# Kernel optimization log

Measured on AMD Instinct MI355X. Metric: run time of the kernel, lower is better.

The kernel has to match this reference:

```python
import jax, jax.numpy as jnp
import numpy as np

N_NODES = 50000
N_EDGES = 800000
D_IN = 64
D_OUT = 64
D_U = 64


def setup_inputs() -> dict:
    key = jax.random.key(0)
    ks = jax.random.split(key, 6)
    x = jax.random.normal(ks[0], (N_NODES, D_IN), dtype=jnp.float32)
    edge_index = jax.random.randint(ks[1], (2, N_EDGES), 0, N_NODES, dtype=jnp.int64)
    edge_weight = jax.random.uniform(ks[2], (N_EDGES,), dtype=jnp.float32)
    u = jax.random.normal(ks[3], (N_NODES, D_U), dtype=jnp.float32)
    # xavier-uniform-like init for W and A
    limW = float(np.sqrt(6.0 / (D_IN + D_OUT)))
    W = jax.random.uniform(ks[4], (D_IN, D_OUT), minval=-limW, maxval=limW, dtype=jnp.float32)
    limA = float(np.sqrt(6.0 / (D_U + D_OUT)))
    A = jax.random.uniform(ks[5], (D_U, D_OUT), minval=-limA, maxval=limA, dtype=jnp.float32)
    bias = jnp.zeros((D_OUT,), dtype=jnp.float32)
    return {"x": x, "edge_index": edge_index, "edge_weight": edge_weight,
            "u": u, "W": W, "A": A, "bias": bias}


def reference(x, edge_index, edge_weight, u, W, A, bias):
    # Non-negative weights via softplus (input-convex constraint)
    W_nn = jax.nn.softplus(W)                      # [D_in, D_out]
    # Transform all nodes once, then gather per edge (equivalent to x[src] @ W per edge)
    h = x @ W_nn                                   # [N, D_out]
    src, dst = edge_index[0], edge_index[1]
    msgs = h[src] * edge_weight[:, None]           # [E, D_out]
    out = jax.ops.segment_sum(msgs, dst, num_segments=x.shape[0])  # [N, D_out]
    out = out + u @ jax.nn.softplus(A) + bias
    return jax.nn.relu(out)
```

## Files before the change

### kernel.cpp

```cpp
#include <hip/hip_runtime.h>

#define NN 50000
#define NE 800000
#define DD 64
#define CAP 64
#define XPAD 68

__global__ void k_softplus(const float* __restrict__ W, const float* __restrict__ A,
                           float* __restrict__ Wnn, float* __restrict__ Ann) {
    int i = blockIdx.x * blockDim.x + threadIdx.x;
    if (i < DD * DD) {
        float w = W[i];
        Wnn[i] = fmaxf(w, 0.f) + log1pf(expf(-fabsf(w)));
        float a = A[i];
        Ann[i] = fmaxf(a, 0.f) + log1pf(expf(-fabsf(a)));
    }
}

__global__ __launch_bounds__(256, 4) void k_transform(
    const float* __restrict__ x, const float* __restrict__ u,
    const float* __restrict__ Wnn, const float* __restrict__ Ann,
    const float* __restrict__ bias,
    float* __restrict__ h, float* __restrict__ base) {
    __shared__ float sW[DD * DD];
    __shared__ float sx[64 * XPAD];

    const int tid = threadIdx.x;
    const int tr = tid >> 4;
    const int tc = tid & 15;
    const int r0 = blockIdx.x * 64;
    const int phase = blockIdx.y;
    const float* __restrict__ in = phase ? u : x;
    const float* __restrict__ wm = phase ? Ann : Wnn;
    float* __restrict__ op = phase ? base : h;
    const int nrow = min(64, NN - r0);

    {
        const float4* w4 = (const float4*)wm;
        float4* sw4 = (float4*)sW;
        #pragma unroll
        for (int i = tid; i < DD * DD / 4; i += 256) sw4[i] = w4[i];
    }
    {
        const float4* x4 = (const float4*)(in + (size_t)r0 * DD);
        const int n4 = nrow * (DD / 4);
        #pragma unroll
        for (int i = tid; i < 64 * (DD / 4); i += 256) {
            float4 v = (i < n4) ? x4[i] : make_float4(0.f, 0.f, 0.f, 0.f);
            *(float4*)&sx[(i >> 4) * XPAD + (i & 15) * 4] = v;
        }
    }
    __syncthreads();

    float4 bv = make_float4(0.f, 0.f, 0.f, 0.f);
    if (phase) bv = *(const float4*)&bias[tc * 4];
    float4 acc[4] = {bv, bv, bv, bv};

    #pragma unroll 4
    for (int k4 = 0; k4 < DD / 4; ++k4) {
        float4 w0 = *(const float4*)&sW[(k4 * 4 + 0) * DD + tc * 4];
        float4 w1 = *(const float4*)&sW[(k4 * 4 + 1) * DD + tc * 4];
        float4 w2 = *(const float4*)&sW[(k4 * 4 + 2) * DD + tc * 4];
        float4 w3 = *(const float4*)&sW[(k4 * 4 + 3) * DD + tc * 4];
        #pragma unroll
        for (int i = 0; i < 4; ++i) {
            float4 xv = *(const float4*)&sx[(tr * 4 + i) * XPAD + k4 * 4];
            acc[i].x += xv.x * w0.x + xv.y * w1.x + xv.z * w2.x + xv.w * w3.x;
            acc[i].y += xv.x * w0.y + xv.y * w1.y + xv.z * w2.y + xv.w * w3.y;
            acc[i].z += xv.x * w0.z + xv.y * w1.z + xv.z * w2.z + xv.w * w3.z;
            acc[i].w += xv.x * w0.w + xv.y * w1.w + xv.z * w2.w + xv.w * w3.w;
        }
    }
    #pragma unroll
    for (int i = 0; i < 4; ++i) {
        int r = r0 + tr * 4 + i;
        if (r < NN) *(float4*)&op[(size_t)r * DD + tc * 4] = acc[i];
    }
}

__global__ __launch_bounds__(256) void k_scatter(
    const int* __restrict__ ei, const float* __restrict__ ew,
    int* __restrict__ cursor, float2* __restrict__ slots) {
    int e = blockIdx.x * 256 + threadIdx.x;
    if (e >= NE) return;
    int s = ei[e];
    int d = ei[NE + e];
    float w = ew[e];
    int pos = atomicAdd(&cursor[d], 1);
    if (pos < CAP) {
        float2 v;
        v.x = __int_as_float(s);
        v.y = w;
        slots[(size_t)d * CAP + pos] = v;
    }
}

__global__ __launch_bounds__(256) void k_apply(
    const int* __restrict__ cursor, const float2* __restrict__ slots,
    const float* __restrict__ h, float* __restrict__ out) {
    int wid = (blockIdx.x * 256 + threadIdx.x) >> 6;
    int lane = threadIdx.x & 63;
    if (wid >= NN) return;
    int deg = min(cursor[wid], CAP);
    const float2* sl = slots + (size_t)wid * CAP;
    float acc = 0.f;
    int i = 0;
    for (; i + 4 <= deg; i += 4) {
        float4 p0 = *(const float4*)(sl + i);
        float4 p1 = *(const float4*)(sl + i + 2);
        int s0 = __float_as_int(p0.x), s1 = __float_as_int(p0.z);
        int s2 = __float_as_int(p1.x), s3 = __float_as_int(p1.z);
        float h0 = h[(size_t)s0 * DD + lane];
        float h1 = h[(size_t)s1 * DD + lane];
        float h2 = h[(size_t)s2 * DD + lane];
        float h3 = h[(size_t)s3 * DD + lane];
        acc += h0 * p0.y + h1 * p0.w + h2 * p1.y + h3 * p1.w;
    }
    for (; i < deg; ++i) {
        float2 v = sl[i];
        acc += h[(size_t)__float_as_int(v.x) * DD + lane] * v.y;
    }
    size_t o = (size_t)wid * DD + lane;
    out[o] = fmaxf(out[o] + acc, 0.f);
}

extern "C" void kernel_launch(void* const* d_in, const int* in_sizes, int n_in,
                              void* d_out, int out_size, void* d_ws, size_t ws_size,
                              hipStream_t stream) {
    const float* x    = (const float*)d_in[0];
    const int*   ei   = (const int*)d_in[1];
    const float* ew   = (const float*)d_in[2];
    const float* u    = (const float*)d_in[3];
    const float* W    = (const float*)d_in[4];
    const float* A    = (const float*)d_in[5];
    const float* bias = (const float*)d_in[6];
    float* out = (float*)d_out;
    float* ws  = (float*)d_ws;

    float* Wnn    = ws;
    float* Ann    = ws + 4096;
    float* h      = ws + 8192;
    int*   cursor = (int*)(ws + 8192 + NN * DD);
    float2* slots = (float2*)(ws + 8192 + NN * DD + NN);

    hipMemsetAsync(cursor, 0, NN * sizeof(int), stream);
    k_softplus<<<(DD * DD + 255) / 256, 256, 0, stream>>>(W, A, Wnn, Ann);
    dim3 tg((NN + 63) / 64, 2);
    k_transform<<<tg, 256, 0, stream>>>(x, u, Wnn, Ann, bias, h, out);
    k_scatter<<<(NE + 255) / 256, 256, 0, stream>>>(ei, ew, cursor, slots);
    k_apply<<<(NN * 64 + 255) / 256, 256, 0, stream>>>(cursor, slots, h, out);
}
```

Before: 186.7 us.

## Fuse softplus, node transform and edge scatter into one kernel launch

Merges the softplus, the dense transform and the edge bucketing scatter into a single kernel. The first blocks do the scatter and the remaining blocks do the transform, with softplus computed inline while the weights load into shared memory. This removes two launches and the intermediate Wnn/Ann buffers, and lets the atomic-heavy scatter overlap with the compute-bound transform. In exchange every transform block recomputes softplus over 4096 weights, scatter blocks carry the 33KB static shared-memory footprint, and the apply kernel gets a tighter launch bound.

New measurement: 203.2 us. +8.8%, slower.

```diff
diff --git a/kernel.cpp b/kernel.cpp
--- a/kernel.cpp
+++ b/kernel.cpp
@@ -5,41 +5,60 @@
 #define DD 64
 #define CAP 64
 #define XPAD 68
+#define NBT 782
+#define NBS 3125
 
-__global__ void k_softplus(const float* __restrict__ W, const float* __restrict__ A,
-                           float* __restrict__ Wnn, float* __restrict__ Ann) {
-    int i = blockIdx.x * blockDim.x + threadIdx.x;
-    if (i < DD * DD) {
-        float w = W[i];
-        Wnn[i] = fmaxf(w, 0.f) + log1pf(expf(-fabsf(w)));
-        float a = A[i];
-        Ann[i] = fmaxf(a, 0.f) + log1pf(expf(-fabsf(a)));
-    }
-}
-
-__global__ __launch_bounds__(256, 4) void k_transform(
+__global__ __launch_bounds__(256, 4) void k_fused(
     const float* __restrict__ x, const float* __restrict__ u,
-    const float* __restrict__ Wnn, const float* __restrict__ Ann,
+    const float* __restrict__ W, const float* __restrict__ A,
     const float* __restrict__ bias,
+    const int* __restrict__ ei, const float* __restrict__ ew,
+    int* __restrict__ cursor, float2* __restrict__ slots,
     float* __restrict__ h, float* __restrict__ base) {
     __shared__ float sW[DD * DD];
     __shared__ float sx[64 * XPAD];
 
     const int tid = threadIdx.x;
+    int b = blockIdx.x;
+
+    if (b < NBS) {
+        int e = b * 256 + tid;
+        if (e < NE) {
+            int s = ei[e];
+            int d = ei[NE + e];
+            float w = ew[e];
+            int pos = atomicAdd(&cursor[d], 1);
+            if (pos < CAP) {
+                float2 v;
+                v.x = __int_as_float(s);
+                v.y = w;
+                slots[(size_t)d * CAP + pos] = v;
+            }
+        }
+        return;
+    }
+    b -= NBS;
+    const int phase = (b >= NBT) ? 1 : 0;
+    const int bx = phase ? b - NBT : b;
+    const float* __restrict__ in = phase ? u : x;
+    const float* __restrict__ wm = phase ? A : W;
+    float* __restrict__ op = phase ? base : h;
+    const int r0 = bx * 64;
+    const int nrow = min(64, NN - r0);
     const int tr = tid >> 4;
     const int tc = tid & 15;
-    const int r0 = blockIdx.x * 64;
-    const int phase = blockIdx.y;
-    const float* __restrict__ in = phase ? u : x;
-    const float* __restrict__ wm = phase ? Ann : Wnn;
-    float* __restrict__ op = phase ? base : h;
-    const int nrow = min(64, NN - r0);
 
     {
         const float4* w4 = (const float4*)wm;
-        float4* sw4 = (float4*)sW;
         #pragma unroll
-        for (int i = tid; i < DD * DD / 4; i += 256) sw4[i] = w4[i];
+        for (int i = tid; i < DD * DD / 4; i += 256) {
+            float4 v = w4[i];
+            v.x = fmaxf(v.x, 0.f) + log1pf(expf(-fabsf(v.x)));
+            v.y = fmaxf(v.y, 0.f) + log1pf(expf(-fabsf(v.y)));
+            v.z = fmaxf(v.z, 0.f) + log1pf(expf(-fabsf(v.z)));
+            v.w = fmaxf(v.w, 0.f) + log1pf(expf(-fabsf(v.w)));
+            *(float4*)&sW[i * 4] = v;
+        }
     }
     {
         const float4* x4 = (const float4*)(in + (size_t)r0 * DD);
@@ -78,24 +97,7 @@
     }
 }
 
-__global__ __launch_bounds__(256) void k_scatter(
-    const int* __restrict__ ei, const float* __restrict__ ew,
-    int* __restrict__ cursor, float2* __restrict__ slots) {
-    int e = blockIdx.x * 256 + threadIdx.x;
-    if (e >= NE) return;
-    int s = ei[e];
-    int d = ei[NE + e];
-    float w = ew[e];
-    int pos = atomicAdd(&cursor[d], 1);
-    if (pos < CAP) {
-        float2 v;
-        v.x = __int_as_float(s);
-        v.y = w;
-        slots[(size_t)d * CAP + pos] = v;
-    }
-}
-
-__global__ __launch_bounds__(256) void k_apply(
+__global__ __launch_bounds__(256, 8) void k_apply(
     const int* __restrict__ cursor, const float2* __restrict__ slots,
     const float* __restrict__ h, float* __restrict__ out) {
     int wid = (blockIdx.x * 256 + threadIdx.x) >> 6;
@@ -137,16 +139,12 @@
     float* out = (float*)d_out;
     float* ws  = (float*)d_ws;
 
-    float* Wnn    = ws;
-    float* Ann    = ws + 4096;
-    float* h      = ws + 8192;
-    int*   cursor = (int*)(ws + 8192 + NN * DD);
-    float2* slots = (float2*)(ws + 8192 + NN * DD + NN);
+    float*  h      = ws;
+    int*    cursor = (int*)(ws + NN * DD);
+    float2* slots  = (float2*)(ws + NN * DD + NN);
 
     hipMemsetAsync(cursor, 0, NN * sizeof(int), stream);
-    k_softplus<<<(DD * DD + 255) / 256, 256, 0, stream>>>(W, A, Wnn, Ann);
-    dim3 tg((NN + 63) / 64, 2);
-    k_transform<<<tg, 256, 0, stream>>>(x, u, Wnn, Ann, bias, h, out);
-    k_scatter<<<(NE + 255) / 256, 256, 0, stream>>>(ei, ew, cursor, slots);
+    k_fused<<<NBS + 2 * NBT, 256, 0, stream>>>(x, u, W, A, bias, ei, ew,
+                                               cursor, slots, h, out);
     k_apply<<<(NN * 64 + 255) / 256, 256, 0, stream>>>(cursor, slots, h, out);
 }
```

## Store transformed node features in bf16 and widen gather unrolling in apply

Applied to the files above, without the earlier changes.

The intermediate h matrix is now written as bf16 instead of fp32, which halves the bytes moved by the random per-edge gathers in the apply kernel. The apply loop is unrolled to 8 edges per iteration with vector slot loads and a 2-edge tail, and it gets a higher occupancy hint. The scatter kernel is launched before the transform, and the bias add is moved after the matmul. The cost is reduced precision in h, which adds rounding error to the aggregated messages.

Measured after the change: 183.8 us. About the same (-1.6%).

```diff
diff --git a/kernel.cpp b/kernel.cpp
--- a/kernel.cpp
+++ b/kernel.cpp
@@ -5,6 +5,15 @@
 #define DD 64
 #define CAP 64
 #define XPAD 68
+
+__device__ __forceinline__ unsigned short f2bf(float f) {
+    unsigned int b = __float_as_uint(f);
+    b += 0x7FFFu + ((b >> 16) & 1u);
+    return (unsigned short)(b >> 16);
+}
+__device__ __forceinline__ float bf2f(unsigned short h) {
+    return __uint_as_float(((unsigned int)h) << 16);
+}
 
 __global__ void k_softplus(const float* __restrict__ W, const float* __restrict__ A,
                            float* __restrict__ Wnn, float* __restrict__ Ann) {
@@ -14,67 +23,6 @@
         Wnn[i] = fmaxf(w, 0.f) + log1pf(expf(-fabsf(w)));
         float a = A[i];
         Ann[i] = fmaxf(a, 0.f) + log1pf(expf(-fabsf(a)));
-    }
-}
-
-__global__ __launch_bounds__(256, 4) void k_transform(
-    const float* __restrict__ x, const float* __restrict__ u,
-    const float* __restrict__ Wnn, const float* __restrict__ Ann,
-    const float* __restrict__ bias,
-    float* __restrict__ h, float* __restrict__ base) {
-    __shared__ float sW[DD * DD];
-    __shared__ float sx[64 * XPAD];
-
-    const int tid = threadIdx.x;
-    const int tr = tid >> 4;
-    const int tc = tid & 15;
-    const int r0 = blockIdx.x * 64;
-    const int phase = blockIdx.y;
-    const float* __restrict__ in = phase ? u : x;
-    const float* __restrict__ wm = phase ? Ann : Wnn;
-    float* __restrict__ op = phase ? base : h;
-    const int nrow = min(64, NN - r0);
-
-    {
-        const float4* w4 = (const float4*)wm;
-        float4* sw4 = (float4*)sW;
-        #pragma unroll
-        for (int i = tid; i < DD * DD / 4; i += 256) sw4[i] = w4[i];
-    }
-    {
-        const float4* x4 = (const float4*)(in + (size_t)r0 * DD);
-        const int n4 = nrow * (DD / 4);
-        #pragma unroll
-        for (int i = tid; i < 64 * (DD / 4); i += 256) {
-            float4 v = (i < n4) ? x4[i] : make_float4(0.f, 0.f, 0.f, 0.f);
-            *(float4*)&sx[(i >> 4) * XPAD + (i & 15) * 4] = v;
-        }
-    }
-    __syncthreads();
-
-    float4 bv = make_float4(0.f, 0.f, 0.f, 0.f);
-    if (phase) bv = *(const float4*)&bias[tc * 4];
-    float4 acc[4] = {bv, bv, bv, bv};
-
-    #pragma unroll 4
-    for (int k4 = 0; k4 < DD / 4; ++k4) {
-        float4 w0 = *(const float4*)&sW[(k4 * 4 + 0) * DD + tc * 4];
-        float4 w1 = *(const float4*)&sW[(k4 * 4 + 1) * DD + tc * 4];
-        float4 w2 = *(const float4*)&sW[(k4 * 4 + 2) * DD + tc * 4];
-        float4 w3 = *(const float4*)&sW[(k4 * 4 + 3) * DD + tc * 4];
-        #pragma unroll
-        for (int i = 0; i < 4; ++i) {
-            float4 xv = *(const float4*)&sx[(tr * 4 + i) * XPAD + k4 * 4];
-            acc[i].x += xv.x * w0.x + xv.y * w1.x + xv.z * w2.x + xv.w * w3.x;
-            acc[i].y += xv.x * w0.y + xv.y * w1.y + xv.z * w2.y + xv.w * w3.y;
-            acc[i].z += xv.x * w0.z + xv.y * w1.z + xv.z * w2.z + xv.w * w3.z;
-            acc[i].w += xv.x * w0.w + xv.y * w1.w + xv.z * w2.w + xv.w * w3.w;
-        }
-    }
-    #pragma unroll
-    for (int i = 0; i < 4; ++i) {
-        int r = r0 + tr * 4 + i;
-        if (r < NN) *(float4*)&op[(size_t)r * DD + tc * 4] = acc[i];
     }
 }
 
@@ -95,30 +43,119 @@
     }
 }
 
-__global__ __launch_bounds__(256) void k_apply(
+__global__ __launch_bounds__(256, 4) void k_transform(
+    const float* __restrict__ x, const float* __restrict__ u,
+    const float* __restrict__ Wnn, const float* __restrict__ Ann,
+    const float* __restrict__ bias,
+    unsigned short* __restrict__ h16, float* __restrict__ out) {
+    __shared__ float sW[DD * DD];
+    __shared__ float sx[64 * XPAD];
+
+    const int tid = threadIdx.x;
+    const int tr = tid >> 4;
+    const int tc = tid & 15;
+    const int r0 = blockIdx.x * 64;
+    const int phase = blockIdx.y;
+    const float* __restrict__ in = phase ? u : x;
+    const float* __restrict__ wm = phase ? Ann : Wnn;
+    const int nrow = min(64, NN - r0);
+
+    {
+        const float4* w4 = (const float4*)wm;
+        float4* sw4 = (float4*)sW;
+        #pragma unroll
+        for (int i = tid; i < DD * DD / 4; i += 256) sw4[i] = w4[i];
+    }
+    {
+        const float4* x4 = (const float4*)(in + (size_t)r0 * DD);
+        const int n4 = nrow * (DD / 4);
+        #pragma unroll
+        for (int i = tid; i < 64 * (DD / 4); i += 256) {
+            float4 v = (i < n4) ? x4[i] : make_float4(0.f, 0.f, 0.f, 0.f);
+            *(float4*)&sx[(i >> 4) * XPAD + (i & 15) * 4] = v;
+        }
+    }
+    __syncthreads();
+
+    float4 acc[4] = {{0,0,0,0},{0,0,0,0},{0,0,0,0},{0,0,0,0}};
+    #pragma unroll 4
+    for (int k4 = 0; k4 < DD / 4; ++k4) {
+        float4 w0 = *(const float4*)&sW[(k4 * 4 + 0) * DD + tc * 4];
+        float4 w1 = *(const float4*)&sW[(k4 * 4 + 1) * DD + tc * 4];
+        float4 w2 = *(const float4*)&sW[(k4 * 4 + 2) * DD + tc * 4];
+        float4 w3 = *(const float4*)&sW[(k4 * 4 + 3) * DD + tc * 4];
+        #pragma unroll
+        for (int i = 0; i < 4; ++i) {
+            float4 xv = *(const float4*)&sx[(tr * 4 + i) * XPAD + k4 * 4];
+            acc[i].x += xv.x * w0.x + xv.y * w1.x + xv.z * w2.x + xv.w * w3.x;
+            acc[i].y += xv.x * w0.y + xv.y * w1.y + xv.z * w2.y + xv.w * w3.y;
+            acc[i].z += xv.x * w0.z + xv.y * w1.z + xv.z * w2.z + xv.w * w3.z;
+            acc[i].w += xv.x * w0.w + xv.y * w1.w + xv.z * w2.w + xv.w * w3.w;
+        }
+    }
+    if (phase) {
+        float4 bv = *(const float4*)&bias[tc * 4];
+        #pragma unroll
+        for (int i = 0; i < 4; ++i) {
+            int r = r0 + tr * 4 + i;
+            if (r < NN) {
+                float4 v = acc[i];
+                v.x += bv.x; v.y += bv.y; v.z += bv.z; v.w += bv.w;
+                *(float4*)&out[(size_t)r * DD + tc * 4] = v;
+            }
+        }
+    } else {
+        #pragma unroll
+        for (int i = 0; i < 4; ++i) {
+            int r = r0 + tr * 4 + i;
+            if (r < NN) {
+                ushort4 hv;
+                hv.x = f2bf(acc[i].x);
+                hv.y = f2bf(acc[i].y);
+                hv.z = f2bf(acc[i].z);
+                hv.w = f2bf(acc[i].w);
+                *(ushort4*)&h16[(size_t)r * DD + tc * 4] = hv;
+            }
+        }
+    }
+}
+
+__global__ __launch_bounds__(256, 8) void k_apply(
     const int* __restrict__ cursor, const float2* __restrict__ slots,
-    const float* __restrict__ h, float* __restrict__ out) {
-    int wid = (blockIdx.x * 256 + threadIdx.x) >> 6;
-    int lane = threadIdx.x & 63;
-    if (wid >= NN) return;
-    int deg = min(cursor[wid], CAP);
-    const float2* sl = slots + (size_t)wid * CAP;
+    const unsigned short* __restrict__ h16, float* __restrict__ out) {
+    const int tid = threadIdx.x;
+    const int wid = (blockIdx.x * 256 + tid) >> 6;
+    const int lane = tid & 63;
+
+    const int deg = min(cursor[wid], CAP);
+    const float4* sl4 = (const float4*)(slots + (size_t)wid * CAP);
     float acc = 0.f;
     int i = 0;
-    for (; i + 4 <= deg; i += 4) {
-        float4 p0 = *(const float4*)(sl + i);
-        float4 p1 = *(const float4*)(sl + i + 2);
-        int s0 = __float_as_int(p0.x), s1 = __float_as_int(p0.z);
-        int s2 = __float_as_int(p1.x), s3 = __float_as_int(p1.z);
-        float h0 = h[(size_t)s0 * DD + lane];
-        float h1 = h[(size_t)s1 * DD + lane];
-        float h2 = h[(size_t)s2 * DD + lane];
-        float h3 = h[(size_t)s3 * DD + lane];
-        acc += h0 * p0.y + h1 * p0.w + h2 * p1.y + h3 * p1.w;
+    for (; i + 8 <= deg; i += 8) {
+        float4 p0 = sl4[(i >> 1) + 0];
+        float4 p1 = sl4[(i >> 1) + 1];
+        float4 p2 = sl4[(i >> 1) + 2];
+        float4 p3 = sl4[(i >> 1) + 3];
+        float h0 = bf2f(h16[(size_t)__float_as_int(p0.x) * DD + lane]);
+        float h1 = bf2f(h16[(size_t)__float_as_int(p0.z) * DD + lane]);
+        float h2 = bf2f(h16[(size_t)__float_as_int(p1.x) * DD + lane]);
+        float h3 = bf2f(h16[(size_t)__float_as_int(p1.z) * DD + lane]);
+        float h4 = bf2f(h16[(size_t)__float_as_int(p2.x) * DD + lane]);
+        float h5 = bf2f(h16[(size_t)__float_as_int(p2.z) * DD + lane]);
+        float h6 = bf2f(h16[(size_t)__float_as_int(p3.x) * DD + lane]);
+        float h7 = bf2f(h16[(size_t)__float_as_int(p3.z) * DD + lane]);
+        acc += h0 * p0.y + h1 * p0.w + h2 * p1.y + h3 * p1.w
+             + h4 * p2.y + h5 * p2.w + h6 * p3.y + h7 * p3.w;
     }
-    for (; i < deg; ++i) {
-        float2 v = sl[i];
-        acc += h[(size_t)__float_as_int(v.x) * DD + lane] * v.y;
+    for (; i + 2 <= deg; i += 2) {
+        float4 p = sl4[i >> 1];
+        float h0 = bf2f(h16[(size_t)__float_as_int(p.x) * DD + lane]);
+        float h1 = bf2f(h16[(size_t)__float_as_int(p.z) * DD + lane]);
+        acc += h0 * p.y + h1 * p.w;
+    }
+    if (i < deg) {
+        float2 ev = slots[(size_t)wid * CAP + i];
+        acc += bf2f(h16[(size_t)__float_as_int(ev.x) * DD + lane]) * ev.y;
     }
     size_t o = (size_t)wid * DD + lane;
     out[o] = fmaxf(out[o] + acc, 0.f);
@@ -137,16 +174,16 @@
     float* out = (float*)d_out;
     float* ws  = (float*)d_ws;
 
-    float* Wnn    = ws;
-    float* Ann    = ws + 4096;
-    float* h      = ws + 8192;
-    int*   cursor = (int*)(ws + 8192 + NN * DD);
-    float2* slots = (float2*)(ws + 8192 + NN * DD + NN);
+    float*          Wnn    = ws;
+    float*          Ann    = ws + 4096;
+    unsigned short* h16    = (unsigned short*)(ws + 8192);
+    int*            cursor = (int*)(ws + 8192 + NN * DD / 2);
+    float2*         slots  = (float2*)(ws + 8192 + NN * DD / 2 + NN);
 
     hipMemsetAsync(cursor, 0, NN * sizeof(int), stream);
     k_softplus<<<(DD * DD + 255) / 256, 256, 0, stream>>>(W, A, Wnn, Ann);
+    k_scatter<<<(NE + 255) / 256, 256, 0, stream>>>(ei, ew, cursor, slots);
     dim3 tg((NN + 63) / 64, 2);
-    k_transform<<<tg, 256, 0, stream>>>(x, u, Wnn, Ann, bias, h, out);
-    k_scatter<<<(NE + 255) / 256, 256, 0, stream>>>(ei, ew, cursor, slots);
-    k_apply<<<(NN * 64 + 255) / 256, 256, 0, stream>>>(cursor, slots, h, out);
+    k_transform<<<tg, 256, 0, stream>>>(x, u, Wnn, Ann, bias, h16, out);
+    k_apply<<<NN / 4, 256, 0, stream>>>(cursor, slots, h16, out);
 }
```
